# Kernel optimization log

Measured on AMD Instinct MI355X. Metric: run time of the kernel, lower is better.

Reference implementation:

```python
import jax, jax.numpy as jnp
import numpy as np

E = 1024        # embedding_dim
H = 16          # num_heads
DR = 1          # downsample_rate
INT = E // DR   # internal_dim
HD = INT // H   # head dim
B, NQ, NK = 4, 2048, 2048


def setup_inputs() -> dict:
    key = jax.random.key(0)
    ks = jax.random.split(key, 11)
    s_in = 1.0 / np.sqrt(E)
    s_int = 1.0 / np.sqrt(INT)
    return {
        "q": jax.random.normal(ks[0], (B, NQ, E), jnp.float32),
        "k": jax.random.normal(ks[1], (B, NK, E), jnp.float32),
        "v": jax.random.normal(ks[2], (B, NK, E), jnp.float32),
        "wq": jax.random.normal(ks[3], (E, INT), jnp.float32) * s_in,
        "bq": jnp.zeros((INT,), jnp.float32),
        "wk": jax.random.normal(ks[4], (E, INT), jnp.float32) * s_in,
        "bk": jnp.zeros((INT,), jnp.float32),
        "wv": jax.random.normal(ks[5], (E, INT), jnp.float32) * s_in,
        "bv": jnp.zeros((INT,), jnp.float32),
        "wo": jax.random.normal(ks[6], (INT, E), jnp.float32) * s_int,
        "bo": jnp.zeros((E,), jnp.float32),
    }


def _heads(x):
    # (B, N, INT) -> (B, H, N, HD)
    b, n, c = x.shape
    return x.reshape(b, n, H, c // H).transpose(0, 2, 1, 3)


def reference(q, k, v, wq, bq, wk, bk, wv, bv, wo, bo):
    qh = _heads(q @ wq + bq)          # (B,H,NQ,HD)
    kh = _heads(k @ wk + bk)          # (B,H,NK,HD)
    vh = _heads(v @ wv + bv)          # (B,H,NK,HD)
    scale = 1.0 / np.sqrt(HD)
    attn = jnp.einsum('bhqd,bhkd->bhqk', qh, kh) * scale  # (B,H,NQ,NK)
    attn = jax.nn.softmax(attn, axis=-1)
    out = jnp.einsum('bhqk,bhkd->bhqd', attn, vh)          # (B,H,NQ,HD)
    out = out.transpose(0, 2, 1, 3).reshape(q.shape[0], qh.shape[2], INT)
    return out @ wo + bo
```

## Files before the change

kernel.cpp:

```cpp
#include <hip/hip_runtime.h>
#include <hip/hip_bf16.h>
#include <cstdint>
#include <cstddef>

typedef __bf16 bf16_t;
typedef __bf16 bf16x8 __attribute__((ext_vector_type(8)));
typedef float f32x4 __attribute__((ext_vector_type(4)));
typedef float f32x16 __attribute__((ext_vector_type(16)));
typedef uint32_t u32;

#define EDIM 1024
#define HH 16
#define HD 64
#define NSEQ 2048
#define QSCALE 0.18033688011f

__device__ __forceinline__ void async_copy16(const bf16_t* gsrc, bf16_t* lds_dst) {
    __builtin_amdgcn_global_load_lds(
        (const __attribute__((address_space(1))) uint32_t*)gsrc,
        (__attribute__((address_space(3))) uint32_t*)lds_dst,
        16, 0, 0);
}

__global__ void cvt_f32_bf16(const float* __restrict__ in, bf16_t* __restrict__ out) {
    size_t i = ((size_t)blockIdx.x * 256 + threadIdx.x) * 8;
    float4 x = *(const float4*)(in + i);
    float4 y = *(const float4*)(in + i + 4);
    bf16x8 v = {(bf16_t)x.x, (bf16_t)x.y, (bf16_t)x.z, (bf16_t)x.w,
                (bf16_t)y.x, (bf16_t)y.y, (bf16_t)y.z, (bf16_t)y.w};
    *(bf16x8*)(out + i) = v;
}

__global__ void transpose_all(const float* __restrict__ w0, const float* __restrict__ w1,
                              const float* __restrict__ w2, const float* __restrict__ w3,
                              bf16_t* __restrict__ o0, bf16_t* __restrict__ o1,
                              bf16_t* __restrict__ o2, bf16_t* __restrict__ o3) {
    __shared__ bf16_t t[64][65];
    const float* in;
    bf16_t* out;
    switch (blockIdx.z) {
        case 0: in = w0; out = o0; break;
        case 1: in = w1; out = o1; break;
        case 2: in = w2; out = o2; break;
        default: in = w3; out = o3; break;
    }
    const int tid = threadIdx.x;
    const int kt = blockIdx.x, nt = blockIdx.y;
    #pragma unroll
    for (int i = 0; i < 16; i++) {
        int idx = i * 256 + tid;
        int r = idx >> 6, c = idx & 63;
        t[r][c] = (bf16_t)in[(size_t)(kt * 64 + r) * 1024 + nt * 64 + c];
    }
    __syncthreads();
    #pragma unroll
    for (int i = 0; i < 16; i++) {
        int idx = i * 256 + tid;
        int r = idx >> 6, c = idx & 63;
        out[(size_t)(nt * 64 + r) * 1024 + kt * 64 + c] = t[c][r];
    }
}

template <int AB, int MODE, typename OUT>
__global__ __launch_bounds__(256, 2)
void gemm_nt(const void* __restrict__ Araw, const bf16_t* __restrict__ Bt,
             const float* __restrict__ bias, OUT* __restrict__ C,
             int M, int N, int K, float oscale) {
    constexpr int BM = 128, BN = 128, BK = 32;
    __shared__ bf16_t Asm[BM * BK];
    __shared__ bf16_t Bsm[BN * BK];
    const int tid = threadIdx.x;
    const int wave = tid >> 6, lane = tid & 63;
    const int quad = lane >> 4, l15 = lane & 15;
    const int n0 = blockIdx.x * BN;
    const int m0 = blockIdx.y * BM;
    const int wm = (wave & 1) * 64, wn = (wave >> 1) * 64;

    f32x4 acc[4][4] = {};

    for (int k0 = 0; k0 < K; k0 += BK) {
        __syncthreads();
        if (AB) {
            const bf16_t* A = (const bf16_t*)Araw;
            #pragma unroll
            for (int i = 0; i < 2; i++) {
                int s = i * 256 + tid;
                int row = s >> 2, c = s & 3;
                int kc = c ^ ((row >> 1) & 3);
                async_copy16(A + (size_t)(m0 + row) * K + k0 + kc * 8, Asm + s * 8);
            }
        } else {
            const float* A = (const float*)Araw;
            #pragma unroll
            for (int i = 0; i < 2; i++) {
                int s = i * 256 + tid;
                int row = s >> 2, c = s & 3;
                int kc = c ^ ((row >> 1) & 3);
                const float* sp = A + (size_t)(m0 + row) * K + k0 + kc * 8;
                float4 x = *(const float4*)sp;
                float4 y = *(const float4*)(sp + 4);
                bf16x8 vv = {(bf16_t)x.x, (bf16_t)x.y, (bf16_t)x.z, (bf16_t)x.w,
                             (bf16_t)y.x, (bf16_t)y.y, (bf16_t)y.z, (bf16_t)y.w};
                *(bf16x8*)&Asm[s * 8] = vv;
            }
        }
        #pragma unroll
        for (int i = 0; i < 2; i++) {
            int s = i * 256 + tid;
            int row = s >> 2, c = s & 3;
            int kc = c ^ ((row >> 1) & 3);
            async_copy16(Bt + (size_t)(n0 + row) * K + k0 + kc * 8, Bsm + s * 8);
        }
        __syncthreads();

        bf16x8 af[4], bfr[4];
        #pragma unroll
        for (int mi = 0; mi < 4; mi++) {
            int row = wm + mi * 16 + l15;
            af[mi] = *(const bf16x8*)&Asm[row * BK + ((quad ^ ((row >> 1) & 3)) * 8)];
        }
        #pragma unroll
        for (int ni = 0; ni < 4; ni++) {
            int row = wn + ni * 16 + l15;
            bfr[ni] = *(const bf16x8*)&Bsm[row * BK + ((quad ^ ((row >> 1) & 3)) * 8)];
        }
        #pragma unroll
        for (int mi = 0; mi < 4; mi++)
            #pragma unroll
            for (int ni = 0; ni < 4; ni++)
                acc[mi][ni] = __builtin_amdgcn_mfma_f32_16x16x32_bf16(
                    af[mi], bfr[ni], acc[mi][ni], 0, 0, 0);
    }

    #pragma unroll
    for (int mi = 0; mi < 4; mi++) {
        #pragma unroll
        for (int ni = 0; ni < 4; ni++) {
            #pragma unroll
            for (int r = 0; r < 4; r++) {
                int m = m0 + wm + mi * 16 + quad * 4 + r;
                int nch = n0 + wn + ni * 16 + l15;
                float v = (acc[mi][ni][r] + bias[nch]) * oscale;
                if (MODE == 2) {
                    C[(size_t)m * N + nch] = (OUT)v;
                } else {
                    int b = m >> 11, n = m & 2047;
                    int h = nch >> 6, d = nch & 63;
                    if (MODE == 0)
                        C[(((size_t)(b * HH + h)) * NSEQ + n) * HD + d] = (OUT)v;
                    else
                        C[(((size_t)(b * HH + h)) * HD + d) * NSEQ + n] = (OUT)v;
                }
            }
        }
    }
}

union PW { u32 w[4]; bf16x8 v; };

__device__ __forceinline__ u32 pack_bf16(float lo, float hi) {
    union { bf16_t h[2]; u32 u; } x;
    x.h[0] = (bf16_t)lo;
    x.h[1] = (bf16_t)hi;
    return x.u;
}

__device__ __forceinline__ void half_swap(u32& a, u32& b) {
    auto r = __builtin_amdgcn_permlane32_swap(a, b, false, false);
    a = r[0];
    b = r[1];
}

__device__ __forceinline__ void softmax_pack(const f32x16 sa, float* lp,
                                             PW& f0, PW& f1) {
    float p[16];
    #pragma unroll
    for (int r = 0; r < 16; r++) {
        p[r] = __builtin_amdgcn_exp2f(sa[r]);
        lp[r & 3] += p[r];
    }
    u32 x0 = pack_bf16(p[0],  p[1]),  x1 = pack_bf16(p[2],  p[3]);
    u32 x2 = pack_bf16(p[4],  p[5]),  x3 = pack_bf16(p[6],  p[7]);
    u32 x4 = pack_bf16(p[8],  p[9]),  x5 = pack_bf16(p[10], p[11]);
    u32 x6 = pack_bf16(p[12], p[13]), x7 = pack_bf16(p[14], p[15]);
    half_swap(x0, x2); half_swap(x1, x3);
    half_swap(x4, x6); half_swap(x5, x7);
    f0.w[0] = x0; f0.w[1] = x1; f0.w[2] = x2; f0.w[3] = x3;
    f1.w[0] = x4; f1.w[1] = x5; f1.w[2] = x6; f1.w[3] = x7;
}

__global__ __launch_bounds__(256, 2)
void attn_kernel(const bf16_t* __restrict__ Qh, const bf16_t* __restrict__ Kh,
                 const bf16_t* __restrict__ Vt, bf16_t* __restrict__ out) {
    __shared__ bf16_t Ks[2][64 * 64];
    __shared__ bf16_t Vs[2][64 * 64];
    const int tid = threadIdx.x, wave = tid >> 6, lane = tid & 63;
    const int l31 = lane & 31, hi = lane >> 5;
    const int B = blockIdx.x;
    const int qt = (B >> 3) & 15;
    const int bh = (B >> 7) * 8 + (B & 7);
    const int b = bh >> 4, h = bh & 15;

    const bf16_t* kbase = Kh + (size_t)bh * NSEQ * HD;
    const bf16_t* vbase = Vt + (size_t)bh * HD * NSEQ;

    bf16x8 qf[4];
    {
        const bf16_t* qrow =
            Qh + ((size_t)bh * NSEQ + qt * 128 + wave * 32 + l31) * HD + hi * 8;
        #pragma unroll
        for (int s = 0; s < 4; s++) qf[s] = *(const bf16x8*)(qrow + s * 16);
    }

    const bf16_t *ks0, *ks1, *vs0, *vs1;
    {
        int r0 = tid >> 3, c0 = tid & 7;
        int s1 = tid + 256;
        int r1 = s1 >> 3, c1 = s1 & 7;
        ks0 = kbase + r0 * HD + (c0 ^ (r0 & 7)) * 8;
        ks1 = kbase + r1 * HD + (c1 ^ (r1 & 7)) * 8;
        vs0 = vbase + (size_t)r0 * NSEQ + (c0 ^ (r0 & 7)) * 8;
        vs1 = vbase + (size_t)r1 * NSEQ + (c1 ^ (r1 & 7)) * 8;
    }

    async_copy16(ks0, &Ks[0][tid * 8]);
    async_copy16(ks1, &Ks[0][(tid + 256) * 8]);
    async_copy16(vs0, &Vs[0][tid * 8]);
    async_copy16(vs1, &Vs[0][(tid + 256) * 8]);

    f32x16 oacc[2] = {};
    float lp[4] = {};

    for (int t = 0; t < 32; t++) {
        const int cur = t & 1;
        __syncthreads();

        if (t < 31) {
            ks0 += 64 * HD; ks1 += 64 * HD;
            vs0 += 64;      vs1 += 64;
            async_copy16(ks0, &Ks[cur ^ 1][tid * 8]);
            async_copy16(ks1, &Ks[cur ^ 1][(tid + 256) * 8]);
            async_copy16(vs0, &Vs[cur ^ 1][tid * 8]);
            async_copy16(vs1, &Vs[cur ^ 1][(tid + 256) * 8]);
        }

        const f32x16 zero = {};
        f32x16 sacc0, sacc1;
        {
            int g = hi;
            int row0 = l31, row1 = 32 + l31;
            bf16x8 ak0 = *(const bf16x8*)&Ks[cur][row0 * 64 + ((g ^ (row0 & 7)) * 8)];
            bf16x8 ak1 = *(const bf16x8*)&Ks[cur][row1 * 64 + ((g ^ (row1 & 7)) * 8)];
            __builtin_amdgcn_s_setprio(1);
            sacc0 = __builtin_amdgcn_mfma_f32_32x32x16_bf16(ak0, qf[0], zero, 0, 0, 0);
            sacc1 = __builtin_amdgcn_mfma_f32_32x32x16_bf16(ak1, qf[0], zero, 0, 0, 0);
            __builtin_amdgcn_s_setprio(0);
        }
        #pragma unroll
        for (int s = 1; s < 4; s++) {
            int g = s * 2 + hi;
            int row0 = l31;
            int row1 = 32 + l31;
            bf16x8 ak0 = *(const bf16x8*)&Ks[cur][row0 * 64 + ((g ^ (row0 & 7)) * 8)];
            bf16x8 ak1 = *(const bf16x8*)&Ks[cur][row1 * 64 + ((g ^ (row1 & 7)) * 8)];
            __builtin_amdgcn_s_setprio(1);
            sacc0 = __builtin_amdgcn_mfma_f32_32x32x16_bf16(ak0, qf[s], sacc0, 0, 0, 0);
            sacc1 = __builtin_amdgcn_mfma_f32_32x32x16_bf16(ak1, qf[s], sacc1, 0, 0, 0);
            __builtin_amdgcn_s_setprio(0);
        }

        PW pa[4];
        softmax_pack(sacc0, lp, pa[0], pa[1]);
        softmax_pack(sacc1, lp, pa[2], pa[3]);

        #pragma unroll
        for (int dt = 0; dt < 2; dt++) {
            #pragma unroll
            for (int ks = 0; ks < 4; ks++) {
                int row = dt * 32 + l31;
                int g = ks * 2 + hi;
                bf16x8 bv = *(const bf16x8*)&Vs[cur][row * 64 + ((g ^ (row & 7)) * 8)];
                __builtin_amdgcn_s_setprio(1);
                oacc[dt] = __builtin_amdgcn_mfma_f32_32x32x16_bf16(
                    pa[ks].v, bv, oacc[dt], 0, 0, 0);
                __builtin_amdgcn_s_setprio(0);
            }
        }
    }

    float lsum = (lp[0] + lp[1]) + (lp[2] + lp[3]);
    lsum += __shfl_xor(lsum, 32, 64);
    float linv = 1.f / lsum;
    float rinv[16];
    #pragma unroll
    for (int r = 0; r < 16; r++) {
        int q = (r & 3) + 8 * (r >> 2) + 4 * hi;
        rinv[r] = __shfl(linv, q, 64);
    }

    const int n0 = qt * 128 + wave * 32;
    #pragma unroll
    for (int dt = 0; dt < 2; dt++) {
        int c = h * 64 + dt * 32 + l31;
        #pragma unroll
        for (int r = 0; r < 16; r++) {
            int q = (r & 3) + 8 * (r >> 2) + 4 * hi;
            out[((size_t)b * NSEQ + n0 + q) * EDIM + c] = (bf16_t)(oacc[dt][r] * rinv[r]);
        }
    }
}

extern "C" void kernel_launch(void* const* d_in, const int* in_sizes, int n_in,
                              void* d_out, int out_size, void* d_ws, size_t ws_size,
                              hipStream_t stream) {
    const float* q  = (const float*)d_in[0];
    const float* k  = (const float*)d_in[1];
    const float* v  = (const float*)d_in[2];
    const float* wq = (const float*)d_in[3];
    const float* bq = (const float*)d_in[4];
    const float* wk = (const float*)d_in[5];
    const float* bk = (const float*)d_in[6];
    const float* wv = (const float*)d_in[7];
    const float* bv = (const float*)d_in[8];
    const float* wo = (const float*)d_in[9];
    const float* bo = (const float*)d_in[10];
    float* out = (float*)d_out;

    char* ws = (char*)d_ws;
    bf16_t* wqt = (bf16_t*)(ws + ((size_t)0  << 20));
    bf16_t* wkt = (bf16_t*)(ws + ((size_t)2  << 20));
    bf16_t* wvt = (bf16_t*)(ws + ((size_t)4  << 20));
    bf16_t* wot = (bf16_t*)(ws + ((size_t)6  << 20));

    const bool big = ws_size >= ((size_t)90 << 20);
    size_t off = big ? ((size_t)24 << 20) : ((size_t)8 << 20);
    bf16_t* X   = (bf16_t*)(ws + ((size_t)8 << 20));
    bf16_t* Qh  = (bf16_t*)(ws + off);
    bf16_t* Kh  = (bf16_t*)(ws + off + ((size_t)16 << 20));
    bf16_t* Vt  = (bf16_t*)(ws + off + ((size_t)32 << 20));
    bf16_t* ao  = (bf16_t*)(ws + off + ((size_t)48 << 20));

    dim3 tb(256);

    transpose_all<<<dim3(16, 16, 4), tb, 0, stream>>>(wq, wk, wv, wo, wqt, wkt, wvt, wot);

    dim3 gg(8, 64);
    if (big) {
        cvt_f32_bf16<<<4096, tb, 0, stream>>>(q, X);
        gemm_nt<1, 0, bf16_t><<<gg, tb, 0, stream>>>(X, wqt, bq, Qh, 8192, 1024, 1024, QSCALE);
        cvt_f32_bf16<<<4096, tb, 0, stream>>>(k, X);
        gemm_nt<1, 0, bf16_t><<<gg, tb, 0, stream>>>(X, wkt, bk, Kh, 8192, 1024, 1024, 1.0f);
        cvt_f32_bf16<<<4096, tb, 0, stream>>>(v, X);
        gemm_nt<1, 1, bf16_t><<<gg, tb, 0, stream>>>(X, wvt, bv, Vt, 8192, 1024, 1024, 1.0f);
    } else {
        gemm_nt<0, 0, bf16_t><<<gg, tb, 0, stream>>>(q, wqt, bq, Qh, 8192, 1024, 1024, QSCALE);
        gemm_nt<0, 0, bf16_t><<<gg, tb, 0, stream>>>(k, wkt, bk, Kh, 8192, 1024, 1024, 1.0f);
        gemm_nt<0, 1, bf16_t><<<gg, tb, 0, stream>>>(v, wvt, bv, Vt, 8192, 1024, 1024, 1.0f);
    }

    attn_kernel<<<1024, tb, 0, stream>>>(Qh, Kh, Vt, ao);

    gemm_nt<1, 2, float><<<gg, tb, 0, stream>>>(ao, wot, bo, out, 8192, 1024, 1024, 1.0f);
}
```

Baseline: 371.2 us.

## Double-buffer projection GEMM with BK=64 and grouped block remapping

The projection GEMM gets two LDS buffers and a doubled K tile of 64, and a new XOR swizzle over 8 chunks. The global-to-LDS copy for the next K tile is issued while the current tile is consumed by MFMAs, to hide load latency and halve the number of barriers. Block indices are remapped so groups of 8 M-tiles share the same N-tile column, which should improve L2 reuse of the weights. LDS use rises to 64KB per block, which may limit occupancy. The float-A path still converts synchronously inside the stage.

```diff
diff --git a/kernel.cpp b/kernel.cpp
--- a/kernel.cpp
+++ b/kernel.cpp
@@ -66,70 +66,84 @@
 void gemm_nt(const void* __restrict__ Araw, const bf16_t* __restrict__ Bt,
              const float* __restrict__ bias, OUT* __restrict__ C,
              int M, int N, int K, float oscale) {
-    constexpr int BM = 128, BN = 128, BK = 32;
-    __shared__ bf16_t Asm[BM * BK];
-    __shared__ bf16_t Bsm[BN * BK];
+    constexpr int BM = 128, BN = 128, BK = 64;
+    __shared__ bf16_t Asm[2][BM * BK];
+    __shared__ bf16_t Bsm[2][BN * BK];
     const int tid = threadIdx.x;
     const int wave = tid >> 6, lane = tid & 63;
     const int quad = lane >> 4, l15 = lane & 15;
-    const int n0 = blockIdx.x * BN;
-    const int m0 = blockIdx.y * BM;
+    const int bx = blockIdx.x, by = blockIdx.y;
+    const int n0 = (by & 7) * BN;
+    const int m0 = ((by >> 3) * 8 + bx) * BM;
     const int wm = (wave & 1) * 64, wn = (wave >> 1) * 64;
 
+    const int srow = tid >> 1;
+    const int NT = K / BK;
+
     f32x4 acc[4][4] = {};
 
-    for (int k0 = 0; k0 < K; k0 += BK) {
-        __syncthreads();
-        if (AB) {
-            const bf16_t* A = (const bf16_t*)Araw;
-            #pragma unroll
-            for (int i = 0; i < 2; i++) {
-                int s = i * 256 + tid;
-                int row = s >> 2, c = s & 3;
-                int kc = c ^ ((row >> 1) & 3);
-                async_copy16(A + (size_t)(m0 + row) * K + k0 + kc * 8, Asm + s * 8);
-            }
-        } else {
-            const float* A = (const float*)Araw;
-            #pragma unroll
-            for (int i = 0; i < 2; i++) {
-                int s = i * 256 + tid;
-                int row = s >> 2, c = s & 3;
-                int kc = c ^ ((row >> 1) & 3);
-                const float* sp = A + (size_t)(m0 + row) * K + k0 + kc * 8;
+    const bf16_t* Ab = (const bf16_t*)Araw;
+    const float* Af = (const float*)Araw;
+
+    auto stage = [&](int t, int buf) {
+        const int k0 = t * BK;
+        #pragma unroll
+        for (int i = 0; i < 4; i++) {
+            int s = i * 256 + tid;
+            int row = s >> 3, c = s & 7;
+            int kc = c ^ (row & 7);
+            if (AB) {
+                async_copy16(Ab + (size_t)(m0 + row) * K + k0 + kc * 8, &Asm[buf][s * 8]);
+            } else {
+                const float* sp = Af + (size_t)(m0 + row) * K + k0 + kc * 8;
                 float4 x = *(const float4*)sp;
                 float4 y = *(const float4*)(sp + 4);
                 bf16x8 vv = {(bf16_t)x.x, (bf16_t)x.y, (bf16_t)x.z, (bf16_t)x.w,
                              (bf16_t)y.x, (bf16_t)y.y, (bf16_t)y.z, (bf16_t)y.w};
-                *(bf16x8*)&Asm[s * 8] = vv;
-            }
-        }
-        #pragma unroll
-        for (int i = 0; i < 2; i++) {
+                *(bf16x8*)&Asm[buf][s * 8] = vv;
+            }
+        }
+        #pragma unroll
+        for (int i = 0; i < 4; i++) {
             int s = i * 256 + tid;
-            int row = s >> 2, c = s & 3;
-            int kc = c ^ ((row >> 1) & 3);
-            async_copy16(Bt + (size_t)(n0 + row) * K + k0 + kc * 8, Bsm + s * 8);
-        }
+            int row = s >> 3, c = s & 7;
+            int kc = c ^ (row & 7);
+            async_copy16(Bt + (size_t)(n0 + row) * K + k0 + kc * 8, &Bsm[buf][s * 8]);
+        }
+    };
+
+    stage(0, 0);
+
+    for (int t = 0; t < NT; t++) {
+        const int buf = t & 1;
         __syncthreads();
 
-        bf16x8 af[4], bfr[4];
-        #pragma unroll
-        for (int mi = 0; mi < 4; mi++) {
-            int row = wm + mi * 16 + l15;
-            af[mi] = *(const bf16x8*)&Asm[row * BK + ((quad ^ ((row >> 1) & 3)) * 8)];
-        }
-        #pragma unroll
-        for (int ni = 0; ni < 4; ni++) {
-            int row = wn + ni * 16 + l15;
-            bfr[ni] = *(const bf16x8*)&Bsm[row * BK + ((quad ^ ((row >> 1) & 3)) * 8)];
-        }
-        #pragma unroll
-        for (int mi = 0; mi < 4; mi++)
-            #pragma unroll
-            for (int ni = 0; ni < 4; ni++)
-                acc[mi][ni] = __builtin_amdgcn_mfma_f32_16x16x32_bf16(
-                    af[mi], bfr[ni], acc[mi][ni], 0, 0, 0);
+        if (t + 1 < NT) stage(t + 1, buf ^ 1);
+
+        bf16x8 af[2][4], bfr[2][4];
+        #pragma unroll
+        for (int ks = 0; ks < 2; ks++) {
+            #pragma unroll
+            for (int mi = 0; mi < 4; mi++) {
+                int row = wm + mi * 16 + l15;
+                int g = ks * 4 + quad;
+                af[ks][mi] = *(const bf16x8*)&Asm[buf][row * BK + ((g ^ (row & 7)) * 8)];
+            }
+            #pragma unroll
+            for (int ni = 0; ni < 4; ni++) {
+                int row = wn + ni * 16 + l15;
+                int g = ks * 4 + quad;
+                bfr[ks][ni] = *(const bf16x8*)&Bsm[buf][row * BK + ((g ^ (row & 7)) * 8)];
+            }
+        }
+        #pragma unroll
+        for (int ks = 0; ks < 2; ks++)
+            #pragma unroll
+            for (int mi = 0; mi < 4; mi++)
+                #pragma unroll
+                for (int ni = 0; ni < 4; ni++)
+                    acc[mi][ni] = __builtin_amdgcn_mfma_f32_16x16x32_bf16(
+                        af[ks][mi], bfr[ks][ni], acc[mi][ni], 0, 0, 0);
     }
 
     #pragma unroll
```

Result: faster. 346.3 us (-6.7%).

## Merge Q/K/V projections into one launch with grouped tile ordering

Applied to the files above, without the earlier changes.

Removes the separate f32-to-bf16 conversion passes and fuses the three input projection GEMMs into a single 1536-block launch that converts f32 activations in-register while loading into LDS. Block indices are remapped so groups of 8 M-tiles share an N column, which is meant to improve L2 reuse of the weight tiles. Launch bounds are raised to 4 blocks per CU. It trades async LDS loads on A for synchronous f32 loads with conversion, and removes the workspace-size branch.

```diff
diff --git a/kernel.cpp b/kernel.cpp
--- a/kernel.cpp
+++ b/kernel.cpp
@@ -20,15 +20,6 @@
         (const __attribute__((address_space(1))) uint32_t*)gsrc,
         (__attribute__((address_space(3))) uint32_t*)lds_dst,
         16, 0, 0);
-}
-
-__global__ void cvt_f32_bf16(const float* __restrict__ in, bf16_t* __restrict__ out) {
-    size_t i = ((size_t)blockIdx.x * 256 + threadIdx.x) * 8;
-    float4 x = *(const float4*)(in + i);
-    float4 y = *(const float4*)(in + i + 4);
-    bf16x8 v = {(bf16_t)x.x, (bf16_t)x.y, (bf16_t)x.z, (bf16_t)x.w,
-                (bf16_t)y.x, (bf16_t)y.y, (bf16_t)y.z, (bf16_t)y.w};
-    *(bf16x8*)(out + i) = v;
 }
 
 __global__ void transpose_all(const float* __restrict__ w0, const float* __restrict__ w1,
@@ -61,48 +52,50 @@
     }
 }
 
-template <int AB, int MODE, typename OUT>
-__global__ __launch_bounds__(256, 2)
-void gemm_nt(const void* __restrict__ Araw, const bf16_t* __restrict__ Bt,
-             const float* __restrict__ bias, OUT* __restrict__ C,
-             int M, int N, int K, float oscale) {
-    constexpr int BM = 128, BN = 128, BK = 32;
+__global__ __launch_bounds__(256, 4)
+void gemm_qkv(const float* __restrict__ Aq, const float* __restrict__ Ak,
+              const float* __restrict__ Av,
+              const bf16_t* __restrict__ Wq, const bf16_t* __restrict__ Wk,
+              const bf16_t* __restrict__ Wv,
+              const float* __restrict__ bq, const float* __restrict__ bk,
+              const float* __restrict__ bv,
+              bf16_t* __restrict__ Qh, bf16_t* __restrict__ Kh,
+              bf16_t* __restrict__ Vt) {
+    constexpr int BM = 128, BN = 128, BK = 32, K = 1024, NT = K / BK;
     __shared__ bf16_t Asm[BM * BK];
     __shared__ bf16_t Bsm[BN * BK];
     const int tid = threadIdx.x;
     const int wave = tid >> 6, lane = tid & 63;
     const int quad = lane >> 4, l15 = lane & 15;
-    const int n0 = blockIdx.x * BN;
-    const int m0 = blockIdx.y * BM;
+    const int bx = blockIdx.x, by = blockIdx.y;
+    const int mt = (by >> 3) * 8 + bx;
+    const int n0 = (by & 7) * BN;
+    const int wt = mt >> 6;
+    const int m0 = (mt - wt * 64) * BM;
     const int wm = (wave & 1) * 64, wn = (wave >> 1) * 64;
 
+    const float*  A    = wt == 0 ? Aq : (wt == 1 ? Ak : Av);
+    const bf16_t* Bt   = wt == 0 ? Wq : (wt == 1 ? Wk : Wv);
+    const float*  bias = wt == 0 ? bq : (wt == 1 ? bk : bv);
+    bf16_t*       Cout = wt == 0 ? Qh : (wt == 1 ? Kh : Vt);
+    const float oscale = wt == 0 ? QSCALE : 1.0f;
+
     f32x4 acc[4][4] = {};
 
-    for (int k0 = 0; k0 < K; k0 += BK) {
+    for (int t = 0; t < NT; t++) {
+        const int k0 = t * BK;
         __syncthreads();
-        if (AB) {
-            const bf16_t* A = (const bf16_t*)Araw;
-            #pragma unroll
-            for (int i = 0; i < 2; i++) {
-                int s = i * 256 + tid;
-                int row = s >> 2, c = s & 3;
-                int kc = c ^ ((row >> 1) & 3);
-                async_copy16(A + (size_t)(m0 + row) * K + k0 + kc * 8, Asm + s * 8);
-            }
-        } else {
-            const float* A = (const float*)Araw;
-            #pragma unroll
-            for (int i = 0; i < 2; i++) {
-                int s = i * 256 + tid;
-                int row = s >> 2, c = s & 3;
-                int kc = c ^ ((row >> 1) & 3);
-                const float* sp = A + (size_t)(m0 + row) * K + k0 + kc * 8;
-                float4 x = *(const float4*)sp;
-                float4 y = *(const float4*)(sp + 4);
-                bf16x8 vv = {(bf16_t)x.x, (bf16_t)x.y, (bf16_t)x.z, (bf16_t)x.w,
-                             (bf16_t)y.x, (bf16_t)y.y, (bf16_t)y.z, (bf16_t)y.w};
-                *(bf16x8*)&Asm[s * 8] = vv;
-            }
+        #pragma unroll
+        for (int i = 0; i < 2; i++) {
+            int s = i * 256 + tid;
+            int row = s >> 2, c = s & 3;
+            int kc = c ^ ((row >> 1) & 3);
+            const float* sp = A + (size_t)(m0 + row) * K + k0 + kc * 8;
+            float4 x = *(const float4*)sp;
+            float4 y = *(const float4*)(sp + 4);
+            bf16x8 vv = {(bf16_t)x.x, (bf16_t)x.y, (bf16_t)x.z, (bf16_t)x.w,
+                         (bf16_t)y.x, (bf16_t)y.y, (bf16_t)y.z, (bf16_t)y.w};
+            *(bf16x8*)&Asm[s * 8] = vv;
         }
         #pragma unroll
         for (int i = 0; i < 2; i++) {
@@ -141,16 +134,80 @@
                 int m = m0 + wm + mi * 16 + quad * 4 + r;
                 int nch = n0 + wn + ni * 16 + l15;
                 float v = (acc[mi][ni][r] + bias[nch]) * oscale;
-                if (MODE == 2) {
-                    C[(size_t)m * N + nch] = (OUT)v;
-                } else {
-                    int b = m >> 11, n = m & 2047;
-                    int h = nch >> 6, d = nch & 63;
-                    if (MODE == 0)
-                        C[(((size_t)(b * HH + h)) * NSEQ + n) * HD + d] = (OUT)v;
-                    else
-                        C[(((size_t)(b * HH + h)) * HD + d) * NSEQ + n] = (OUT)v;
-                }
+                int b = m >> 11, n = m & 2047;
+                int h = nch >> 6, d = nch & 63;
+                if (wt < 2)
+                    Cout[(((size_t)(b * HH + h)) * NSEQ + n) * HD + d] = (bf16_t)v;
+                else
+                    Cout[(((size_t)(b * HH + h)) * HD + d) * NSEQ + n] = (bf16_t)v;
+            }
+        }
+    }
+}
+
+__global__ __launch_bounds__(256, 4)
+void gemm_out(const bf16_t* __restrict__ A, const bf16_t* __restrict__ Bt,
+              const float* __restrict__ bias, float* __restrict__ C) {
+    constexpr int BM = 128, BN = 128, BK = 32, K = 1024, N = 1024, NT = K / BK;
+    __shared__ bf16_t Asm[BM * BK];
+    __shared__ bf16_t Bsm[BN * BK];
+    const int tid = threadIdx.x;
+    const int wave = tid >> 6, lane = tid & 63;
+    const int quad = lane >> 4, l15 = lane & 15;
+    const int bx = blockIdx.x, by = blockIdx.y;
+    const int n0 = (by & 7) * BN;
+    const int m0 = ((by >> 3) * 8 + bx) * BM;
+    const int wm = (wave & 1) * 64, wn = (wave >> 1) * 64;
+
+    f32x4 acc[4][4] = {};
+
+    for (int t = 0; t < NT; t++) {
+        const int k0 = t * BK;
+        __syncthreads();
+        #pragma unroll
+        for (int i = 0; i < 2; i++) {
+            int s = i * 256 + tid;
+            int row = s >> 2, c = s & 3;
+            int kc = c ^ ((row >> 1) & 3);
+            async_copy16(A + (size_t)(m0 + row) * K + k0 + kc * 8, Asm + s * 8);
+        }
+        #pragma unroll
+        for (int i = 0; i < 2; i++) {
+            int s = i * 256 + tid;
+            int row = s >> 2, c = s & 3;
+            int kc = c ^ ((row >> 1) & 3);
+            async_copy16(Bt + (size_t)(n0 + row) * K + k0 + kc * 8, Bsm + s * 8);
+        }
+        __syncthreads();
+
+        bf16x8 af[4], bfr[4];
+        #pragma unroll
+        for (int mi = 0; mi < 4; mi++) {
+            int row = wm + mi * 16 + l15;
+            af[mi] = *(const bf16x8*)&Asm[row * BK + ((quad ^ ((row >> 1) & 3)) * 8)];
+        }
+        #pragma unroll
+        for (int ni = 0; ni < 4; ni++) {
+            int row = wn + ni * 16 + l15;
+            bfr[ni] = *(const bf16x8*)&Bsm[row * BK + ((quad ^ ((row >> 1) & 3)) * 8)];
+        }
+        #pragma unroll
+        for (int mi = 0; mi < 4; mi++)
+            #pragma unroll
+            for (int ni = 0; ni < 4; ni++)
+                acc[mi][ni] = __builtin_amdgcn_mfma_f32_16x16x32_bf16(
+                    af[mi], bfr[ni], acc[mi][ni], 0, 0, 0);
+    }
+
+    #pragma unroll
+    for (int mi = 0; mi < 4; mi++) {
+        #pragma unroll
+        for (int ni = 0; ni < 4; ni++) {
+            #pragma unroll
+            for (int r = 0; r < 4; r++) {
+                int m = m0 + wm + mi * 16 + quad * 4 + r;
+                int nch = n0 + wn + ni * 16 + l15;
+                C[(size_t)m * N + nch] = acc[mi][ni][r] + bias[nch];
             }
         }
     }
@@ -332,33 +389,19 @@
     bf16_t* wvt = (bf16_t*)(ws + ((size_t)4  << 20));
     bf16_t* wot = (bf16_t*)(ws + ((size_t)6  << 20));
 
-    const bool big = ws_size >= ((size_t)90 << 20);
-    size_t off = big ? ((size_t)24 << 20) : ((size_t)8 << 20);
-    bf16_t* X   = (bf16_t*)(ws + ((size_t)8 << 20));
-    bf16_t* Qh  = (bf16_t*)(ws + off);
-    bf16_t* Kh  = (bf16_t*)(ws + off + ((size_t)16 << 20));
-    bf16_t* Vt  = (bf16_t*)(ws + off + ((size_t)32 << 20));
-    bf16_t* ao  = (bf16_t*)(ws + off + ((size_t)48 << 20));
+    bf16_t* Qh  = (bf16_t*)(ws + ((size_t)8  << 20));
+    bf16_t* Kh  = (bf16_t*)(ws + ((size_t)24 << 20));
+    bf16_t* Vt  = (bf16_t*)(ws + ((size_t)40 << 20));
+    bf16_t* ao  = (bf16_t*)(ws + ((size_t)56 << 20));
 
     dim3 tb(256);
 
     transpose_all<<<dim3(16, 16, 4), tb, 0, stream>>>(wq, wk, wv, wo, wqt, wkt, wvt, wot);
 
-    dim3 gg(8, 64);
-    if (big) {
-        cvt_f32_bf16<<<4096, tb, 0, stream>>>(q, X);
-        gemm_nt<1, 0, bf16_t><<<gg, tb, 0, stream>>>(X, wqt, bq, Qh, 8192, 1024, 1024, QSCALE);
-        cvt_f32_bf16<<<4096, tb, 0, stream>>>(k, X);
-        gemm_nt<1, 0, bf16_t><<<gg, tb, 0, stream>>>(X, wkt, bk, Kh, 8192, 1024, 1024, 1.0f);
-        cvt_f32_bf16<<<4096, tb, 0, stream>>>(v, X);
-        gemm_nt<1, 1, bf16_t><<<gg, tb, 0, stream>>>(X, wvt, bv, Vt, 8192, 1024, 1024, 1.0f);
-    } else {
-        gemm_nt<0, 0, bf16_t><<<gg, tb, 0, stream>>>(q, wqt, bq, Qh, 8192, 1024, 1024, QSCALE);
-        gemm_nt<0, 0, bf16_t><<<gg, tb, 0, stream>>>(k, wkt, bk, Kh, 8192, 1024, 1024, 1.0f);
-        gemm_nt<0, 1, bf16_t><<<gg, tb, 0, stream>>>(v, wvt, bv, Vt, 8192, 1024, 1024, 1.0f);
-    }
+    gemm_qkv<<<dim3(8, 192), tb, 0, stream>>>(q, k, v, wqt, wkt, wvt,
+                                              bq, bk, bv, Qh, Kh, Vt);
 
     attn_kernel<<<1024, tb, 0, stream>>>(Qh, Kh, Vt, ao);
 
-    gemm_nt<1, 2, float><<<gg, tb, 0, stream>>>(ao, wot, bo, out, 8192, 1024, 1024, 1.0f);
-}
+    gemm_out<<<dim3(8, 64), tb, 0, stream>>>(ao, wot, bo, out);
+}
```

After: 374.7 us. About the same (+1.0%).
